# Optimization experiments

Measured on AMD Instinct MI355X. Metric: run time of the kernel, lower is better.

Reference implementation:

```python
import jax, jax.numpy as jnp
import numpy as np

D_MODEL = 1024
N_HEADS = 16
HEAD_DIM = D_MODEL // N_HEADS
BATCH = 1
SEQLEN = 4096


def setup_inputs() -> dict:
    key = jax.random.key(0)
    k1, k2, k3 = jax.random.split(key, 3)
    x = jax.random.normal(k1, (BATCH, SEQLEN, D_MODEL), dtype=jnp.float32)
    # match typical Dense init scale so softmax isn't saturated
    Wqkv = jax.random.normal(k2, (D_MODEL, 3 * D_MODEL), dtype=jnp.float32) / np.sqrt(D_MODEL)
    Wout = jax.random.normal(k3, (D_MODEL, D_MODEL), dtype=jnp.float32) / np.sqrt(D_MODEL)
    return {"x": x, "Wqkv": Wqkv, "Wout": Wout}


def reference(x, Wqkv, Wout):
    b, l, d = x.shape
    qkv = x @ Wqkv  # [b, l, 3d]
    q, k, v = jnp.split(qkv, 3, axis=-1)
    # [b, l, d] -> [b, h, l, hd]
    def to_heads(t):
        return t.reshape(b, l, N_HEADS, HEAD_DIM).transpose(0, 2, 1, 3)
    q, k, v = to_heads(q), to_heads(k), to_heads(v)
    scale = 1.0 / np.sqrt(HEAD_DIM)
    attn = jnp.einsum('bhld,bhsd->bhls', q, k) * scale  # [b,h,l,l]
    causal_mask = jnp.tril(jnp.ones((l, l), dtype=bool))
    attn = jnp.where(causal_mask, attn, -jnp.inf)
    attn = jax.nn.softmax(attn, axis=-1)
    out = jnp.einsum('bhls,bhsd->bhld', attn, v)  # [b,h,l,hd]
    out = out.transpose(0, 2, 1, 3).reshape(b, l, d)
    return out @ Wout
```

## Files before the change

kernel.cpp:

```cpp
#include <hip/hip_runtime.h>

#define SEQ 4096
#define DM 1024
#define NH 16
#define HD 64

typedef __attribute__((ext_vector_type(8))) short short8;
typedef __attribute__((ext_vector_type(4))) short short4v;
typedef __attribute__((ext_vector_type(2))) short short2v;
typedef __attribute__((ext_vector_type(4))) float float4v;
typedef __attribute__((ext_vector_type(4))) int int4v;

__device__ __forceinline__ short f2bf(float f) {
    union { float f; unsigned u; } v; v.f = f;
    unsigned u = v.u;
    return (short)((u + 0x7fffu + ((u >> 16) & 1u)) >> 16);
}
__device__ __forceinline__ int pk2bf(float a, float b) {
    union { float f; unsigned u; } x, y; x.f = a; y.f = b;
    return (int)__builtin_amdgcn_perm(y.u + 0x8000u, x.u + 0x8000u, 0x07060302u);
}

__device__ __forceinline__ void gload_lds16(const void* g, void* l) {
    __builtin_amdgcn_global_load_lds(
        (const __attribute__((address_space(1))) void*)g,
        (__attribute__((address_space(3))) void*)l, 16, 0, 0);
}

__global__ __launch_bounds__(256) void prep_kernel(const float* __restrict__ x,
                                                   const float* __restrict__ Wqkv,
                                                   const float* __restrict__ Wout,
                                                   short* __restrict__ xb,
                                                   short* __restrict__ wqkvT,
                                                   short* __restrict__ woutT,
                                                   float qscale) {
    __shared__ float tile[32][33];
    int id = blockIdx.x;
    int tid = threadIdx.x;
    if (id < 4096) {
        int i = id * 256 + tid;
        float4v v = ((const float4v*)x)[i];
        short4v o;
        o[0] = f2bf(v[0]); o[1] = f2bf(v[1]); o[2] = f2bf(v[2]); o[3] = f2bf(v[3]);
        ((short4v*)xb)[i] = o;
        return;
    }
    const float* in; short* outp; int H, W, sr; float sc; int gx, gy;
    if (id < 4096 + 3072) {
        int i2 = id - 4096;
        in = Wqkv; outp = wqkvT; H = DM; W = 3 * DM; sr = DM; sc = qscale;
        gx = i2 % 96; gy = i2 / 96;
    } else {
        int i3 = id - 7168;
        in = Wout; outp = woutT; H = DM; W = DM; sr = 0; sc = 1.0f;
        gx = i3 % 32; gy = i3 / 32;
    }
    int bx = gx * 32, by = gy * 32;
    int tx = tid & 31, ty = tid >> 5;
#pragma unroll
    for (int i = 0; i < 32; i += 8)
        tile[ty + i][tx] = in[(by + ty + i) * W + bx + tx];
    __syncthreads();
#pragma unroll
    for (int i = 0; i < 32; i += 8) {
        int orow = bx + ty + i;
        float s = (orow < sr) ? sc : 1.0f;
        outp[orow * H + by + tx] = f2bf(tile[tx][ty + i] * s);
    }
}

__global__ __launch_bounds__(256) void gemm_qkv(const short* __restrict__ A,
                                                const short* __restrict__ BT,
                                                short* __restrict__ C,
                                                short* __restrict__ vt) {
    const int K = DM, N = 3 * DM;
    __shared__ short As[128 * 32];
    __shared__ short Bs[128 * 32];
    __shared__ short Vt[64 * 136];
    int tid  = threadIdx.x;
    int m0   = blockIdx.y * 128;
    int n0   = blockIdx.x * 128;
    int w    = tid >> 6, lane = tid & 63;
    int wm   = w >> 1,  wn   = w & 1;
    int quad = lane >> 4, l15 = lane & 15;
    int srow = lane >> 2;
    int scol = (lane & 3) * 8;

    float4v acc[4][4];
#pragma unroll
    for (int mi = 0; mi < 4; mi++)
#pragma unroll
        for (int ni = 0; ni < 4; ni++)
            acc[mi][ni] = {0.f, 0.f, 0.f, 0.f};

    for (int k0 = 0; k0 < K; k0 += 32) {
        __syncthreads();
#pragma unroll
        for (int t = 0; t < 2; t++) {
            int chunk = w * 2 + t;
            int r = chunk * 16 + srow;
            gload_lds16(&A[(m0 + r) * K + k0 + scol], &As[chunk * 16 * 32]);
            gload_lds16(&BT[(n0 + r) * K + k0 + scol], &Bs[chunk * 16 * 32]);
        }
        __syncthreads();
        short8 a[4], b[4];
#pragma unroll
        for (int mi = 0; mi < 4; mi++)
            a[mi] = *(const short8*)&As[(wm * 64 + mi * 16 + l15) * 32 + quad * 8];
#pragma unroll
        for (int ni = 0; ni < 4; ni++)
            b[ni] = *(const short8*)&Bs[(wn * 64 + ni * 16 + l15) * 32 + quad * 8];
#pragma unroll
        for (int mi = 0; mi < 4; mi++)
#pragma unroll
            for (int ni = 0; ni < 4; ni++)
                acc[mi][ni] = __builtin_amdgcn_mfma_f32_16x16x32_bf16(a[mi], b[ni], acc[mi][ni], 0, 0, 0);
    }

    if (n0 < 2 * DM) {
#pragma unroll
        for (int mi = 0; mi < 4; mi++)
#pragma unroll
            for (int ni = 0; ni < 4; ni++)
#pragma unroll
                for (int r = 0; r < 4; r++) {
                    int row = m0 + wm * 64 + mi * 16 + quad * 4 + r;
                    int col = n0 + wn * 64 + ni * 16 + l15;
                    C[row * N + col] = f2bf(acc[mi][ni][r]);
                }
    } else {
#pragma unroll
        for (int half = 0; half < 2; half++) {
            __syncthreads();
            if (wn == half) {
#pragma unroll
                for (int mi = 0; mi < 4; mi++)
#pragma unroll
                    for (int ni = 0; ni < 4; ni++) {
                        int drow  = ni * 16 + l15;
                        int sbase = wm * 64 + mi * 16 + quad * 4;
                        short4v pv;
#pragma unroll
                        for (int r = 0; r < 4; r++)
                            pv[r] = f2bf(acc[mi][ni][r]);
                        *(short4v*)&Vt[drow * 136 + sbase] = pv;
                    }
            }
            __syncthreads();
#pragma unroll
            for (int p = 0; p < 4; p++) {
                int drow  = p * 16 + (tid >> 4);
                int chunk = tid & 15;
                int sl    = chunk * 8;
                int sg    = m0 + sl;
                int swz0  = (sg & ~31) | ((sg & 12) << 1) | ((sg & 16) >> 2);
                int sg1   = sg + 4;
                int swz1  = (sg1 & ~31) | ((sg1 & 12) << 1) | ((sg1 & 16) >> 2);
                int dcolg = n0 - 2 * DM + half * 64 + drow;
                short4v a0 = *(const short4v*)&Vt[drow * 136 + sl];
                short4v a1 = *(const short4v*)&Vt[drow * 136 + sl + 4];
                *(short4v*)&vt[dcolg * SEQ + swz0] = a0;
                *(short4v*)&vt[dcolg * SEQ + swz1] = a1;
            }
        }
    }
}

__global__ __launch_bounds__(256) void gemm_bt64(const short* __restrict__ A,
                                                 const short* __restrict__ BT,
                                                 float* __restrict__ C,
                                                 int M, int N, int K) {
    __shared__ short As[64 * 32];
    __shared__ short Bs[128 * 32];
    int tid  = threadIdx.x;
    int m0   = blockIdx.y * 64;
    int n0   = blockIdx.x * 128;
    int w    = tid >> 6, lane = tid & 63;
    int wm   = w >> 1,  wn   = w & 1;
    int quad = lane >> 4, l15 = lane & 15;
    int srow = lane >> 2;
    int scol = (lane & 3) * 8;

    float4v acc[2][4];
#pragma unroll
    for (int mi = 0; mi < 2; mi++)
#pragma unroll
        for (int ni = 0; ni < 4; ni++)
            acc[mi][ni] = {0.f, 0.f, 0.f, 0.f};

    for (int k0 = 0; k0 < K; k0 += 32) {
        __syncthreads();
        {
            int r = w * 16 + srow;
            gload_lds16(&A[(m0 + r) * K + k0 + scol], &As[w * 16 * 32]);
        }
#pragma unroll
        for (int t = 0; t < 2; t++) {
            int chunk = w * 2 + t;
            int r = chunk * 16 + srow;
            gload_lds16(&BT[(n0 + r) * K + k0 + scol], &Bs[chunk * 16 * 32]);
        }
        __syncthreads();
        short8 a[2], b[4];
#pragma unroll
        for (int mi = 0; mi < 2; mi++)
            a[mi] = *(const short8*)&As[(wm * 32 + mi * 16 + l15) * 32 + quad * 8];
#pragma unroll
        for (int ni = 0; ni < 4; ni++)
            b[ni] = *(const short8*)&Bs[(wn * 64 + ni * 16 + l15) * 32 + quad * 8];
#pragma unroll
        for (int mi = 0; mi < 2; mi++)
#pragma unroll
            for (int ni = 0; ni < 4; ni++)
                acc[mi][ni] = __builtin_amdgcn_mfma_f32_16x16x32_bf16(a[mi], b[ni], acc[mi][ni], 0, 0, 0);
    }

#pragma unroll
    for (int mi = 0; mi < 2; mi++)
#pragma unroll
        for (int ni = 0; ni < 4; ni++)
#pragma unroll
            for (int r = 0; r < 4; r++) {
                int row = m0 + wm * 32 + mi * 16 + quad * 4 + r;
                int col = n0 + wn * 64 + ni * 16 + l15;
                C[row * N + col] = acc[mi][ni][r];
            }
}

__global__ __launch_bounds__(256) void attn_kernel(const short* __restrict__ qkv,
                                                   const short* __restrict__ vtp,
                                                   short* __restrict__ aout) {
    __shared__ short Ks[64 * 72];
    __shared__ short Vs[64 * 72];
    int h = blockIdx.x;
    int y = blockIdx.y;
    int t = (y < 16) ? (31 - y) : (y - 16);
    int q0 = t * 128;
    int tid = threadIdx.x;
    int w = tid >> 6, lane = tid & 63;
    int quad = lane >> 4, l15 = lane & 15;
    int qw = q0 + w * 32;
    int r8 = lane >> 3, c8 = lane & 7;
    int srow = w * 16 + r8;

    const short* Kg = qkv + DM + h * HD;
    const short* Vg = vtp + (h * HD) * SEQ;

    short8 aq[2][2];
#pragma unroll
    for (int mi = 0; mi < 2; mi++)
#pragma unroll
        for (int kk = 0; kk < 2; kk++)
            aq[mi][kk] = *(const short8*)&qkv[(qw + mi * 16 + l15) * (3 * DM) + h * HD + kk * 32 + quad * 8];

    float lp[2] = {0.f, 0.f};
    float4v o[2][4];
#pragma unroll
    for (int mi = 0; mi < 2; mi++)
#pragma unroll
        for (int dt = 0; dt < 4; dt++)
            o[mi][dt] = {0.f, 0.f, 0.f, 0.f};

    int nTblk = 2 * t + 2;

    short8 kg[2], vg[2];
#pragma unroll
    for (int i = 0; i < 2; i++) {
        kg[i] = *(const short8*)&Kg[(srow + 8 * i) * (3 * DM) + c8 * 8];
        vg[i] = *(const short8*)&Vg[(srow + 8 * i) * SEQ + c8 * 8];
    }

    for (int tt = 0; tt < nTblk; tt++) {
        int s0 = tt * 64;
        int sn = (tt + 1 < nTblk) ? s0 + 64 : s0;

        __syncthreads();
#pragma unroll
        for (int i = 0; i < 2; i++) {
            *(short8*)&Ks[(srow + 8 * i) * 72 + c8 * 8] = kg[i];
            *(short8*)&Vs[(srow + 8 * i) * 72 + c8 * 8] = vg[i];
        }
#pragma unroll
        for (int i = 0; i < 2; i++) {
            kg[i] = *(const short8*)&Kg[(sn + srow + 8 * i) * (3 * DM) + c8 * 8];
            vg[i] = *(const short8*)&Vg[(srow + 8 * i) * SEQ + sn + c8 * 8];
        }
        __syncthreads();

        short8 kc[8], vc[8];
#pragma unroll
        for (int ni = 0; ni < 4; ni++)
#pragma unroll
            for (int kk = 0; kk < 2; kk++)
                kc[ni * 2 + kk] = *(const short8*)&Ks[(ni * 16 + l15) * 72 + kk * 32 + quad * 8];
#pragma unroll
        for (int dt = 0; dt < 4; dt++)
#pragma unroll
            for (int pr = 0; pr < 2; pr++)
                vc[dt * 2 + pr] = *(const short8*)&Vs[(dt * 16 + l15) * 72 + pr * 32 + quad * 8];

        float4v s[2][4];
#pragma unroll
        for (int mi = 0; mi < 2; mi++)
#pragma unroll
            for (int ni = 0; ni < 4; ni++) {
                float4v a = {0.f, 0.f, 0.f, 0.f};
#pragma unroll
                for (int kk = 0; kk < 2; kk++)
                    a = __builtin_amdgcn_mfma_f32_16x16x32_bf16(kc[ni * 2 + kk], aq[mi][kk], a, 0, 0, 0);
                s[mi][ni] = a;
            }

        bool diag = (s0 + 63 > qw);
        short8 pa[2][2];
#pragma unroll
        for (int mi = 0; mi < 2; mi++) {
            int qrow = qw + mi * 16 + l15;
#pragma unroll
            for (int ni = 0; ni < 4; ni++) {
#pragma unroll
                for (int r = 0; r < 4; r++) {
                    float p = __builtin_amdgcn_exp2f(s[mi][ni][r]);
                    if (diag) {
                        int scol = s0 + ni * 16 + quad * 4 + r;
                        p = (scol <= qrow) ? p : 0.f;
                    }
                    lp[mi] += p;
                    s[mi][ni][r] = p;
                }
            }
#pragma unroll
            for (int pr = 0; pr < 2; pr++) {
                int4v wpk;
                wpk[0] = pk2bf(s[mi][2 * pr][0], s[mi][2 * pr][1]);
                wpk[1] = pk2bf(s[mi][2 * pr][2], s[mi][2 * pr][3]);
                wpk[2] = pk2bf(s[mi][2 * pr + 1][0], s[mi][2 * pr + 1][1]);
                wpk[3] = pk2bf(s[mi][2 * pr + 1][2], s[mi][2 * pr + 1][3]);
                pa[mi][pr] = *(short8*)&wpk;
            }
        }
#pragma unroll
        for (int mi = 0; mi < 2; mi++)
#pragma unroll
            for (int dt = 0; dt < 4; dt++)
#pragma unroll
                for (int pr = 0; pr < 2; pr++)
                    o[mi][dt] = __builtin_amdgcn_mfma_f32_16x16x32_bf16(pa[mi][pr], vc[dt * 2 + pr], o[mi][dt], 0, 0, 0);
    }

#pragma unroll
    for (int mi = 0; mi < 2; mi++) {
        lp[mi] += __shfl_xor(lp[mi], 16, 64);
        lp[mi] += __shfl_xor(lp[mi], 32, 64);
    }
#pragma unroll
    for (int mi = 0; mi < 2; mi++)
#pragma unroll
        for (int r = 0; r < 4; r++) {
            float lr = __shfl(lp[mi], quad * 4 + r, 16);
            float inv = 1.0f / lr;
#pragma unroll
            for (int dt = 0; dt < 4; dt++) {
                float v = o[mi][dt][r] * inv;
                aout[(qw + mi * 16 + quad * 4 + r) * DM + h * HD + dt * 16 + l15] = f2bf(v);
            }
        }
}

extern "C" void kernel_launch(void* const* d_in, const int* in_sizes, int n_in,
                              void* d_out, int out_size, void* d_ws, size_t ws_size,
                              hipStream_t stream) {
    const float* x    = (const float*)d_in[0];
    const float* Wqkv = (const float*)d_in[1];
    const float* Wout = (const float*)d_in[2];
    float* out = (float*)d_out;

    char* ws = (char*)d_ws;
    short* xb    = (short*)(ws);
    short* wqkvT = (short*)(ws + 8388608);
    short* woutT = (short*)(ws + 8388608 + 6291456);
    short* qkv   = (short*)(ws + 16777216);
    short* vt    = (short*)(ws + 16777216 + 25165824);
    short* ao    = (short*)(ws + 16777216 + 25165824 + 8388608);

    const float SC = 0.18033688011112042f;

    prep_kernel<<<8192, 256, 0, stream>>>(x, Wqkv, Wout, xb, wqkvT, woutT, SC);

    gemm_qkv<<<dim3(3 * DM / 128, SEQ / 128), 256, 0, stream>>>(xb, wqkvT, qkv, vt);

    attn_kernel<<<dim3(NH, SEQ / 128), 256, 0, stream>>>(qkv, vt, ao);

    gemm_bt64<<<dim3(DM / 128, SEQ / 64), 256, 0, stream>>>(ao, woutT, out, SEQ, DM, DM);
}
```

Measured before the change: 224.3 us.

## Double-buffer attention K/V tiles via async global-to-LDS loads with swizzle

Rewrites the attention kernel to use 128-thread blocks over 64-query tiles, giving twice as many blocks with a reordered causal schedule. K/V tiles are staged with direct global-to-LDS loads into double buffers, and an XOR swizzle replaces the padded layout. This drops the register staging and one barrier per iteration, aiming to overlap loads with MFMA work and improve load balance. Risks include less K/V reuse per block and correctness depending on when the async LDS loads complete relative to the single barrier.

Measured after the change: 235.4 us. 5.0% more time.

```diff
diff --git a/kernel.cpp b/kernel.cpp
--- a/kernel.cpp
+++ b/kernel.cpp
@@ -227,21 +227,23 @@
             }
 }
 
-__global__ __launch_bounds__(256) void attn_kernel(const short* __restrict__ qkv,
+__global__ __launch_bounds__(128) void attn_kernel(const short* __restrict__ qkv,
                                                    const short* __restrict__ vtp,
                                                    short* __restrict__ aout) {
-    __shared__ short Ks[64 * 72];
-    __shared__ short Vs[64 * 72];
+    __shared__ short Ks[2][64 * 64];
+    __shared__ short Vs[2][64 * 64];
     int h = blockIdx.x;
     int y = blockIdx.y;
-    int t = (y < 16) ? (31 - y) : (y - 16);
-    int q0 = t * 128;
+    int j = y & 15, g = y >> 4;
+    int t = (g == 0) ? 63 - j : (g == 1) ? j : (g == 2) ? 47 - j : 16 + j;
+    int q0 = t * 64;
     int tid = threadIdx.x;
     int w = tid >> 6, lane = tid & 63;
     int quad = lane >> 4, l15 = lane & 15;
+    int x7 = l15 & 7;
     int qw = q0 + w * 32;
-    int r8 = lane >> 3, c8 = lane & 7;
-    int srow = w * 16 + r8;
+    int sr = lane >> 3;
+    int sc = (lane & 7) ^ (sr & 7);
 
     const short* Kg = qkv + DM + h * HD;
     const short* Vg = vtp + (h * HD) * SEQ;
@@ -261,44 +263,42 @@
         for (int dt = 0; dt < 4; dt++)
             o[mi][dt] = {0.f, 0.f, 0.f, 0.f};
 
-    int nTblk = 2 * t + 2;
-
-    short8 kg[2], vg[2];
-#pragma unroll
-    for (int i = 0; i < 2; i++) {
-        kg[i] = *(const short8*)&Kg[(srow + 8 * i) * (3 * DM) + c8 * 8];
-        vg[i] = *(const short8*)&Vg[(srow + 8 * i) * SEQ + c8 * 8];
-    }
-
-    for (int tt = 0; tt < nTblk; tt++) {
+    int nT = t + 1;
+
+#pragma unroll
+    for (int seg = 0; seg < 4; seg++) {
+        int rb = w * 32 + seg * 8;
+        gload_lds16(&Kg[(rb + sr) * (3 * DM) + sc * 8], &Ks[0][rb * 64]);
+        gload_lds16(&Vg[(rb + sr) * SEQ + sc * 8], &Vs[0][rb * 64]);
+    }
+    __syncthreads();
+
+    for (int tt = 0; tt < nT; tt++) {
+        int cur = tt & 1;
+        if (tt + 1 < nT) {
+            int sn = (tt + 1) * 64;
+#pragma unroll
+            for (int seg = 0; seg < 4; seg++) {
+                int rb = w * 32 + seg * 8;
+                gload_lds16(&Kg[(sn + rb + sr) * (3 * DM) + sc * 8], &Ks[cur ^ 1][rb * 64]);
+                gload_lds16(&Vg[(rb + sr) * SEQ + sn + sc * 8], &Vs[cur ^ 1][rb * 64]);
+            }
+        }
+        const short* Kc = Ks[cur];
+        const short* Vc = Vs[cur];
+        short8 kc[8], vc[8];
+#pragma unroll
+        for (int ni = 0; ni < 4; ni++)
+#pragma unroll
+            for (int kk = 0; kk < 2; kk++)
+                kc[ni * 2 + kk] = *(const short8*)&Kc[(ni * 16 + l15) * 64 + ((quad + 4 * kk) ^ x7) * 8];
+#pragma unroll
+        for (int dt = 0; dt < 4; dt++)
+#pragma unroll
+            for (int pr = 0; pr < 2; pr++)
+                vc[dt * 2 + pr] = *(const short8*)&Vc[(dt * 16 + l15) * 64 + ((quad + 4 * pr) ^ x7) * 8];
+
         int s0 = tt * 64;
-        int sn = (tt + 1 < nTblk) ? s0 + 64 : s0;
-
-        __syncthreads();
-#pragma unroll
-        for (int i = 0; i < 2; i++) {
-            *(short8*)&Ks[(srow + 8 * i) * 72 + c8 * 8] = kg[i];
-            *(short8*)&Vs[(srow + 8 * i) * 72 + c8 * 8] = vg[i];
-        }
-#pragma unroll
-        for (int i = 0; i < 2; i++) {
-            kg[i] = *(const short8*)&Kg[(sn + srow + 8 * i) * (3 * DM) + c8 * 8];
-            vg[i] = *(const short8*)&Vg[(srow + 8 * i) * SEQ + sn + c8 * 8];
-        }
-        __syncthreads();
-
-        short8 kc[8], vc[8];
-#pragma unroll
-        for (int ni = 0; ni < 4; ni++)
-#pragma unroll
-            for (int kk = 0; kk < 2; kk++)
-                kc[ni * 2 + kk] = *(const short8*)&Ks[(ni * 16 + l15) * 72 + kk * 32 + quad * 8];
-#pragma unroll
-        for (int dt = 0; dt < 4; dt++)
-#pragma unroll
-            for (int pr = 0; pr < 2; pr++)
-                vc[dt * 2 + pr] = *(const short8*)&Vs[(dt * 16 + l15) * 72 + pr * 32 + quad * 8];
-
         float4v s[2][4];
 #pragma unroll
         for (int mi = 0; mi < 2; mi++)
@@ -346,6 +346,7 @@
 #pragma unroll
                 for (int pr = 0; pr < 2; pr++)
                     o[mi][dt] = __builtin_amdgcn_mfma_f32_16x16x32_bf16(pa[mi][pr], vc[dt * 2 + pr], o[mi][dt], 0, 0, 0);
+        __syncthreads();
     }
 
 #pragma unroll
@@ -389,7 +390,7 @@
 
     gemm_qkv<<<dim3(3 * DM / 128, SEQ / 128), 256, 0, stream>>>(xb, wqkvT, qkv, vt);
 
-    attn_kernel<<<dim3(NH, SEQ / 128), 256, 0, stream>>>(qkv, vt, ao);
+    attn_kernel<<<dim3(NH, SEQ / 64), 128, 0, stream>>>(qkv, vt, ao);
 
     gemm_bt64<<<dim3(DM / 128, SEQ / 64), 256, 0, stream>>>(ao, woutT, out, SEQ, DM, DM);
 }
```
